# Performance work log

Hardware: AMD Instinct MI355X
Metric: run time of the kernel (lower is better)

The kernel has to match this reference:

```python
import jax, jax.numpy as jnp
import numpy as np

B, LQ, LK, D = 16, 32, 256, 512
H, DK = 8, 64
LN_EPS = 1e-5


def _layernorm(x, g, b):
    m = jnp.mean(x, axis=-1, keepdims=True)
    var = jnp.mean(jnp.square(x - m), axis=-1, keepdims=True)
    return (x - m) * jax.lax.rsqrt(var + LN_EPS) * g + b


def setup_inputs() -> dict:
    key = jax.random.key(0)
    ks = jax.random.split(key, 10)
    s = 0.02
    return {
        "q": jax.random.normal(ks[0], (B, LQ, D), jnp.float32),
        "k": jax.random.normal(ks[1], (B, LK, D), jnp.float32),
        "v": jax.random.normal(ks[2], (B, LK, D), jnp.float32),
        "Wq": jax.random.normal(ks[3], (D, D), jnp.float32) * s,
        "Wk": jax.random.normal(ks[4], (D, D), jnp.float32) * s,
        "Wv": jax.random.normal(ks[5], (D, D), jnp.float32) * s,
        "Wfc": jax.random.normal(ks[6], (D, D), jnp.float32) * s,
        "Wg": jax.random.normal(ks[7], (2 * D, D), jnp.float32) * s,
        "bg": jnp.zeros((2 * D,), jnp.float32),
        "Wvp": jax.random.normal(ks[8], (D, D), jnp.float32) * s,
        "bvp": jnp.zeros((D,), jnp.float32),
        "ln1_g": jnp.ones((D,), jnp.float32),
        "ln1_b": jnp.zeros((D,), jnp.float32),
        "ln2_g": jnp.ones((D,), jnp.float32),
        "ln2_b": jnp.zeros((D,), jnp.float32),
    }


def reference(q, k, v, Wq, Wk, Wv, Wfc, Wg, bg, Wvp, bvp, ln1_g, ln1_b, ln2_g, ln2_b):
    # FiLM parameters from queries: [B, LQ, 2D] -> tanh gammas/betas [B, LQ, D]
    film = q @ Wg.T + bg
    gammas, betas = jnp.split(film, 2, axis=-1)
    gammas = jnp.tanh(gammas)
    betas = jnp.tanh(betas)
    # Visual conditioning base: LN(vis_proj(k)) -> [B, LK, D]
    cond_base = _layernorm(k @ Wvp.T + bvp, ln1_g, ln1_b)
    # Per-query modulated keys: broadcast instead of repeat -> [B, LQ, LK, D]
    cond = gammas[:, :, None, :] * cond_base[:, None, :, :] + betas[:, :, None, :]
    cond_k = k[:, None, :, :] + _layernorm(cond, ln2_g, ln2_b)
    # Projections (torch Linear: y = x @ W^T), no qkv bias
    qh = (q @ Wq.T).reshape(B, LQ, H, DK)                 # [B, LQ, H, DK]
    kh = (cond_k @ Wk.T).reshape(B, LQ, LK, H, DK)        # [B, LQ, LK, H, DK]
    vh = (cond_k @ Wv.T).reshape(B, LQ, LK, H, DK)
    # Per-query attention over LK (note: forward arg `v` is unused, as in original)
    scale = DK ** (-0.5)
    logits = jnp.einsum("blhd,blkhd->bhlk", qh, kh) * scale
    weights = jax.nn.softmax(logits, axis=-1)
    # attn_drop/proj_drop are identity in eval mode
    attn = jnp.einsum("bhlk,blkhd->blhd", weights, vh).reshape(B, LQ, H * DK)
    return attn @ Wfc.T
```

## Files before the change

### kernel.cpp

```cpp
#include <hip/hip_runtime.h>
#include <math.h>

namespace {
constexpr float LN_EPS = 1e-5f;

typedef unsigned short u16;
typedef __attribute__((ext_vector_type(8))) short bh8;
typedef __attribute__((ext_vector_type(4))) float fv4;

__device__ __forceinline__ float4 ld4(const float* p) { return *reinterpret_cast<const float4*>(p); }

__device__ __forceinline__ float b2f(u16 x) {
  union { float f; unsigned u; } c; c.u = ((unsigned)x) << 16; return c.f;
}
__device__ __forceinline__ u16 f2b(float f) {
  union { float f; unsigned u; } c; c.f = f;
  unsigned u = c.u;
  u += 0x7FFFu + ((u >> 16) & 1u);
  return (u16)(u >> 16);
}
__device__ __forceinline__ unsigned pk2(float a, float b) {
  return (unsigned)f2b(a) | ((unsigned)f2b(b) << 16);
}
__device__ __forceinline__ uint4 pack8(const float* v) {
  uint4 r; r.x = pk2(v[0], v[1]); r.y = pk2(v[2], v[3]); r.z = pk2(v[4], v[5]); r.w = pk2(v[6], v[7]);
  return r;
}

__device__ __forceinline__ bh8 lds_rd(const u16* S, int row, int c8) {
  return *(const bh8*)&S[row * 64 + ((c8 ^ (row & 7)) << 3)];
}

struct FA {
  const float *q, *k, *Wq, *Wk, *Wv, *Wfc, *Wg, *bg, *Wvp, *bvp;
  const float *ln1g, *ln1b, *ln2g, *ln2b;
  float* out;
  u16 *WkT_bf, *Wv_bf, *Wfc_bf, *k_bf, *kT_bf, *qh_bf;
  float *gam, *bet, *condpre;
  u16 *cb_bf, *cbT_bf, *u_bf, *w1_bf;
  float *c2, *c3, *c4;
  u16* A96_bf;
  float *sum_be, *sum_be2, *P;
  u16* s_bf;
  u16 *cbsq_bf, *w_bf, *W1_bf;
  float *S1, *S2;
  u16* attn_bf;
  float *K1, *K2;
};

struct GA {
  const u16* A; const u16* B; const u16* Balt;
  long lda, ldb, sAz, sBz;
  float* Cf; u16* Cb; u16* Cb2;
  long ldc, sCz;
  int M, K, epi;
  const float* e0; const float* e1;
};

__device__ __forceinline__ void gemm_core(const GA& a, u16* As, u16* Bs,
                                          int bx, int by, int bz, int t) {
  const int z = bz;
  const int bm0 = bx * 64, bn0 = by * 64;
  const int lane = t & 63, w = t >> 6;
  const int wm = (w >> 1) * 32, wn = (w & 1) * 32;
  const u16* Ab = a.A + (long)z * a.sAz;
  const u16* Bbase = (a.Balt != nullptr && bm0 >= 64) ? a.Balt : a.B;
  const u16* Bb = Bbase + (long)z * a.sBz;

  const int sr = t >> 3, sc8 = t & 7, sc = sc8 * 8;
  int ar0 = bm0 + sr;      if (ar0 > a.M - 1) ar0 = a.M - 1;
  int ar1 = bm0 + sr + 32; if (ar1 > a.M - 1) ar1 = a.M - 1;
  const u16* ap0 = Ab + (long)ar0 * a.lda + sc;
  const u16* ap1 = Ab + (long)ar1 * a.lda + sc;
  const u16* bp0 = Bb + (long)(bn0 + sr) * a.ldb + sc;
  const u16* bp1 = Bb + (long)(bn0 + sr + 32) * a.ldb + sc;
  const int iA0 = sr * 64 + ((sc8 ^ (sr & 7)) << 3);
  const int iA1 = iA0 + 32 * 64;

  fv4 zero = {0.f, 0.f, 0.f, 0.f};
  fv4 acc00 = zero, acc01 = zero, acc10 = zero, acc11 = zero;
  const int r0 = lane & 15, kq8 = lane >> 4;
  const int nk = a.K >> 6;

  uint4 av0 = *(const uint4*)ap0, av1 = *(const uint4*)ap1;
  uint4 bv0 = *(const uint4*)bp0, bv1 = *(const uint4*)bp1;
  for (int kt = 0; kt < nk; ++kt) {
    __syncthreads();
    *(uint4*)&As[iA0] = av0; *(uint4*)&As[iA1] = av1;
    *(uint4*)&Bs[iA0] = bv0; *(uint4*)&Bs[iA1] = bv1;
    __syncthreads();
    if (kt + 1 < nk) {
      ap0 += 64; ap1 += 64; bp0 += 64; bp1 += 64;
      av0 = *(const uint4*)ap0; av1 = *(const uint4*)ap1;
      bv0 = *(const uint4*)bp0; bv1 = *(const uint4*)bp1;
    }
#pragma unroll
    for (int kc = 0; kc < 2; ++kc) {
      const int c8 = kq8 + 4 * kc;
      bh8 aa0 = lds_rd(As, wm + r0, c8);
      bh8 aa1 = lds_rd(As, wm + 16 + r0, c8);
      bh8 bb0 = lds_rd(Bs, wn + r0, c8);
      bh8 bb1 = lds_rd(Bs, wn + 16 + r0, c8);
      acc00 = __builtin_amdgcn_mfma_f32_16x16x32_bf16(aa0, bb0, acc00, 0, 0, 0);
      acc01 = __builtin_amdgcn_mfma_f32_16x16x32_bf16(aa0, bb1, acc01, 0, 0, 0);
      acc10 = __builtin_amdgcn_mfma_f32_16x16x32_bf16(aa1, bb0, acc10, 0, 0, 0);
      acc11 = __builtin_amdgcn_mfma_f32_16x16x32_bf16(aa1, bb1, acc11, 0, 0, 0);
    }
  }

  fv4 accs[2][2] = {{acc00, acc01}, {acc10, acc11}};
#pragma unroll
  for (int rb = 0; rb < 2; ++rb) {
#pragma unroll
    for (int cbl = 0; cbl < 2; ++cbl) {
#pragma unroll
      for (int j = 0; j < 4; ++j) {
        const int r = bm0 + wm + rb * 16 + (lane >> 4) * 4 + j;
        const int c = bn0 + wn + cbl * 16 + (lane & 15);
        if (r >= a.M) continue;
        const float v = accs[rb][cbl][j];
        if (a.epi == 0) {
          a.Cf[(long)z * a.sCz + (long)r * a.ldc + c] = v;
        } else if (a.epi == 1) {
          a.Cb[(long)z * a.sCz + (long)r * a.ldc + c] = f2b(v);
        } else if (a.epi == 5) {
          a.Cb[((long)r * 8 + z) * a.ldc + c] = f2b(v * 0.125f);
        } else {
          const u16 ub = f2b(v * 0.125f);
          const long orow = (long)r * 8 + z;
          a.Cb[orow * 512 + c] = ub;
          const float uu = b2f(ub);
          const float t1 = a.e1[c] * uu;
          a.Cb2[orow * 512 + c] = f2b(a.e0[(long)r * 512 + c] * t1);
        }
      }
    }
  }
}

struct GAF {
  const float* Af; const float* Bf;
  long lda, ldb;
  float* Cf; u16* Cb; float* Cf2;
  long ldc;
  int M, K, epi;
  const float* e0;
};

__device__ __forceinline__ void gemm_core_f32(const GAF& a, u16* As, u16* Bs,
                                              int bx, int by, int t) {
  const int bm0 = bx * 64, bn0 = by * 64;
  const int lane = t & 63, w = t >> 6;
  const int wm = (w >> 1) * 32, wn = (w & 1) * 32;
  const int sr = t >> 3, sc8 = t & 7, sc = sc8 * 8;
  int ar0 = bm0 + sr;      if (ar0 > a.M - 1) ar0 = a.M - 1;
  int ar1 = bm0 + sr + 32; if (ar1 > a.M - 1) ar1 = a.M - 1;
  const float* ap0 = a.Af + (long)ar0 * a.lda + sc;
  const float* ap1 = a.Af + (long)ar1 * a.lda + sc;
  const float* bp0 = a.Bf + (long)(bn0 + sr) * a.ldb + sc;
  const float* bp1 = a.Bf + (long)(bn0 + sr + 32) * a.ldb + sc;
  const int iA0 = sr * 64 + ((sc8 ^ (sr & 7)) << 3);
  const int iA1 = iA0 + 32 * 64;

  fv4 zero = {0.f, 0.f, 0.f, 0.f};
  fv4 acc00 = zero, acc01 = zero, acc10 = zero, acc11 = zero;
  const int r0 = lane & 15, kq8 = lane >> 4;
  const int nk = a.K >> 6;

  float4 xa0 = ld4(ap0), xa1 = ld4(ap0 + 4), xa2 = ld4(ap1), xa3 = ld4(ap1 + 4);
  float4 xb0 = ld4(bp0), xb1 = ld4(bp0 + 4), xb2 = ld4(bp1), xb3 = ld4(bp1 + 4);
  for (int kt = 0; kt < nk; ++kt) {
    __syncthreads();
    {
      const float v0[8] = {xa0.x, xa0.y, xa0.z, xa0.w, xa1.x, xa1.y, xa1.z, xa1.w};
      const float v1[8] = {xa2.x, xa2.y, xa2.z, xa2.w, xa3.x, xa3.y, xa3.z, xa3.w};
      const float v2[8] = {xb0.x, xb0.y, xb0.z, xb0.w, xb1.x, xb1.y, xb1.z, xb1.w};
      const float v3[8] = {xb2.x, xb2.y, xb2.z, xb2.w, xb3.x, xb3.y, xb3.z, xb3.w};
      *(uint4*)&As[iA0] = pack8(v0);
      *(uint4*)&As[iA1] = pack8(v1);
      *(uint4*)&Bs[iA0] = pack8(v2);
      *(uint4*)&Bs[iA1] = pack8(v3);
    }
    __syncthreads();
    if (kt + 1 < nk) {
      ap0 += 64; ap1 += 64; bp0 += 64; bp1 += 64;
      xa0 = ld4(ap0); xa1 = ld4(ap0 + 4); xa2 = ld4(ap1); xa3 = ld4(ap1 + 4);
      xb0 = ld4(bp0); xb1 = ld4(bp0 + 4); xb2 = ld4(bp1); xb3 = ld4(bp1 + 4);
    }
#pragma unroll
    for (int kc = 0; kc < 2; ++kc) {
      const int c8 = kq8 + 4 * kc;
      bh8 aa0 = lds_rd(As, wm + r0, c8);
      bh8 aa1 = lds_rd(As, wm + 16 + r0, c8);
      bh8 bb0 = lds_rd(Bs, wn + r0, c8);
      bh8 bb1 = lds_rd(Bs, wn + 16 + r0, c8);
      acc00 = __builtin_amdgcn_mfma_f32_16x16x32_bf16(aa0, bb0, acc00, 0, 0, 0);
      acc01 = __builtin_amdgcn_mfma_f32_16x16x32_bf16(aa0, bb1, acc01, 0, 0, 0);
      acc10 = __builtin_amdgcn_mfma_f32_16x16x32_bf16(aa1, bb0, acc10, 0, 0, 0);
      acc11 = __builtin_amdgcn_mfma_f32_16x16x32_bf16(aa1, bb1, acc11, 0, 0, 0);
    }
  }

  fv4 accs[2][2] = {{acc00, acc01}, {acc10, acc11}};
#pragma unroll
  for (int rb = 0; rb < 2; ++rb) {
#pragma unroll
    for (int cbl = 0; cbl < 2; ++cbl) {
#pragma unroll
      for (int j = 0; j < 4; ++j) {
        const int r = bm0 + wm + rb * 16 + (lane >> 4) * 4 + j;
        const int c = bn0 + wn + cbl * 16 + (lane & 15);
        if (r >= a.M) continue;
        const float v = accs[rb][cbl][j];
        if (a.epi == 1) {
          a.Cb[(long)r * a.ldc + c] = f2b(v);
        } else if (a.epi == 2) {
          const float x = tanhf(v + a.e0[c]);
          if (c < 512) a.Cf[(long)r * 512 + c] = x;
          else         a.Cf2[(long)r * 512 + (c - 512)] = x;
        } else {
          a.Cf[(long)r * a.ldc + c] = v + a.e0[c];
        }
      }
    }
  }
}

struct GA2 {
  const u16* A1; const u16* A2; const u16* B1; const u16* B2;
  long lda, ldb, sAz, sBz;
  float* Cf; float* Cf2; u16* Cb;
  long ldc, sCz;
  int M, K;
  const float* e1; const float* e2; const float* e3;
  const float* e4; const float* e5; const float* e6;
};

__device__ __forceinline__ void gemm2_core(const GA2& a, u16* As1, u16* As2,
                                           u16* Bs1, u16* Bs2,
                                           int bx, int by, int bz, int t, int EPI) {
  const int z = bz;
  const int bm0 = bx * 64, bn0 = by * 64;
  const int lane = t & 63, w = t >> 6;
  const int wm = (w >> 1) * 32, wn = (w & 1) * 32;
  const u16* A1b = a.A1 + (long)z * a.sAz;
  const u16* A2b = a.A2 + (long)z * a.sAz;
  const u16* B1b = a.B1 + (long)z * a.sBz;
  const u16* B2b = a.B2 + (long)z * a.sBz;

  const int sr = t >> 3, sc8 = t & 7, sc = sc8 * 8;
  const long aoff0 = (long)(bm0 + sr) * a.lda + sc;
  const long aoff1 = (long)(bm0 + sr + 32) * a.lda + sc;
  const long boff0 = (long)(bn0 + sr) * a.ldb + sc;
  const long boff1 = (long)(bn0 + sr + 32) * a.ldb + sc;
  const u16 *a1p0 = A1b + aoff0, *a1p1 = A1b + aoff1;
  const u16 *a2p0 = A2b + aoff0, *a2p1 = A2b + aoff1;
  const u16 *b1p0 = B1b + boff0, *b1p1 = B1b + boff1;
  const u16 *b2p0 = B2b + boff0, *b2p1 = B2b + boff1;
  const int iA0 = sr * 64 + ((sc8 ^ (sr & 7)) << 3);
  const int iA1 = iA0 + 32 * 64;

  fv4 zero = {0.f, 0.f, 0.f, 0.f};
  fv4 p00 = zero, p01 = zero, p10 = zero, p11 = zero;
  fv4 q00 = zero, q01 = zero, q10 = zero, q11 = zero;
  const int r0 = lane & 15, kq8 = lane >> 4;
  const int nk = a.K >> 6;

  uint4 a1v0 = *(const uint4*)a1p0, a1v1 = *(const uint4*)a1p1;
  uint4 a2v0 = *(const uint4*)a2p0, a2v1 = *(const uint4*)a2p1;
  uint4 b1v0 = *(const uint4*)b1p0, b1v1 = *(const uint4*)b1p1;
  uint4 b2v0 = *(const uint4*)b2p0, b2v1 = *(const uint4*)b2p1;
  for (int kt = 0; kt < nk; ++kt) {
    __syncthreads();
    *(uint4*)&As1[iA0] = a1v0; *(uint4*)&As1[iA1] = a1v1;
    *(uint4*)&As2[iA0] = a2v0; *(uint4*)&As2[iA1] = a2v1;
    *(uint4*)&Bs1[iA0] = b1v0; *(uint4*)&Bs1[iA1] = b1v1;
    *(uint4*)&Bs2[iA0] = b2v0; *(uint4*)&Bs2[iA1] = b2v1;
    __syncthreads();
    if (kt + 1 < nk) {
      a1p0 += 64; a1p1 += 64; a2p0 += 64; a2p1 += 64;
      b1p0 += 64; b1p1 += 64; b2p0 += 64; b2p1 += 64;
      a1v0 = *(const uint4*)a1p0; a1v1 = *(const uint4*)a1p1;
      a2v0 = *(const uint4*)a2p0; a2v1 = *(const uint4*)a2p1;
      b1v0 = *(const uint4*)b1p0; b1v1 = *(const uint4*)b1p1;
      b2v0 = *(const uint4*)b2p0; b2v1 = *(const uint4*)b2p1;
    }
#pragma unroll
    for (int kc = 0; kc < 2; ++kc) {
      const int c8 = kq8 + 4 * kc;
      bh8 x0 = lds_rd(As1, wm + r0, c8);
      bh8 x1 = lds_rd(As1, wm + 16 + r0, c8);
      bh8 y0 = lds_rd(Bs1, wn + r0, c8);
      bh8 y1 = lds_rd(Bs1, wn + 16 + r0, c8);
      p00 = __builtin_amdgcn_mfma_f32_16x16x32_bf16(x0, y0, p00, 0, 0, 0);
      p01 = __builtin_amdgcn_mfma_f32_16x16x32_bf16(x0, y1, p01, 0, 0, 0);
      p10 = __builtin_amdgcn_mfma_f32_16x16x32_bf16(x1, y0, p10, 0, 0, 0);
      p11 = __builtin_amdgcn_mfma_f32_16x16x32_bf16(x1, y1, p11, 0, 0, 0);
      bh8 u0 = lds_rd(As2, wm + r0, c8);
      bh8 u1 = lds_rd(As2, wm + 16 + r0, c8);
      bh8 v0 = lds_rd(Bs2, wn + r0, c8);
      bh8 v1 = lds_rd(Bs2, wn + 16 + r0, c8);
      q00 = __builtin_amdgcn_mfma_f32_16x16x32_bf16(u0, v0, q00, 0, 0, 0);
      q01 = __builtin_amdgcn_mfma_f32_16x16x32_bf16(u0, v1, q01, 0, 0, 0);
      q10 = __builtin_amdgcn_mfma_f32_16x16x32_bf16(u1, v0, q10, 0, 0, 0);
      q11 = __builtin_amdgcn_mfma_f32_16x16x32_bf16(u1, v1, q11, 0, 0, 0);
    }
  }

  fv4 pa[2][2] = {{p00, p01}, {p10, p11}};
  fv4 qa[2][2] = {{q00, q01}, {q10, q11}};
#pragma unroll
  for (int rb = 0; rb < 2; ++rb) {
#pragma unroll
    for (int cbl = 0; cbl < 2; ++cbl) {
#pragma unroll
      for (int j = 0; j < 4; ++j) {
        const int r = bm0 + wm + rb * 16 + (lane >> 4) * 4 + j;
        const int c = bn0 + wn + cbl * 16 + (lane & 15);
        if (r >= a.M) continue;
        const float v1 = pa[rb][cbl][j];
        const float v2 = qa[rb][cbl][j];
        if (EPI == 2) {
          const long idx = (long)z * a.sCz + (long)r * a.ldc + c;
          a.Cf[idx] = v1;
          a.Cf2[idx] = v2;
        } else {
          const int lh = z * 256 + r;
          const int bl = z * 32 + (r >> 3);
          const float G2d = a.e1[c], B2d = a.e2[c];
          const float gv = a.e3[(long)bl * 512 + c];
          const float bev = a.e4[(long)bl * 512 + c];
          const float sv = v1 + B2d + G2d * (gv * v2 + bev * a.e5[lh] - a.e6[lh]);
          a.Cb[(long)z * a.sCz + (long)r * a.ldc + c] = f2b(sv);
        }
      }
    }
  }
}

__device__ __forceinline__ void tpf32_unit(const float* src, long lds, u16* dst, long ldd,
                                           int tr, int tc, int t, float T[64][65]) {
  const int c = t & 63, rg = t >> 6;
#pragma unroll 4
  for (int i = 0; i < 16; ++i) {
    const int r = rg + 4 * i;
    T[r][c] = src[(long)(tr * 64 + r) * lds + tc * 64 + c];
  }
  __syncthreads();
#pragma unroll 4
  for (int i = 0; i < 16; ++i) {
    const int r = rg + 4 * i;
    dst[(long)(tc * 64 + r) * ldd + tr * 64 + c] = f2b(T[c][r]);
  }
}

__device__ __forceinline__ void tpb16_unit(const u16* src, u16* dst, int b, int w32,
                                           int t, float T[64][65]) {
  const int tr = w32 >> 3, tc = w32 & 7;
  const u16* s = src + (long)b * 131072;
  u16* d = dst + (long)b * 131072;
  const int c = t & 63, rg = t >> 6;
#pragma unroll 4
  for (int i = 0; i < 16; ++i) {
    const int r = rg + 4 * i;
    T[r][c] = b2f(s[(long)(tr * 64 + r) * 512 + tc * 64 + c]);
  }
  __syncthreads();
#pragma unroll 4
  for (int i = 0; i < 16; ++i) {
    const int r = rg + 4 * i;
    d[(long)(tc * 64 + r) * 256 + tr * 64 + c] = f2b(T[c][r]);
  }
}

__device__ __forceinline__ void cvt_unit(const float* s, u16* d, long blk, int t) {
  const long idx = blk * 2048 + t * 8;
  const float4 x0 = ld4(s + idx), x1 = ld4(s + idx + 4);
  const float v[8] = {x0.x, x0.y, x0.z, x0.w, x1.x, x1.y, x1.z, x1.w};
  *(uint4*)(d + idx) = pack8(v);
}

__device__ __forceinline__ void ln_unit(const FA& f, int u, int t) {
  const int lane = t & 63, e = lane * 8;
  const int row = u * 4 + (t >> 6);
  const float* p = f.condpre + (long)row * 512 + e;
  const float4 x0 = ld4(p), x1 = ld4(p + 4);
  float v[8] = {x0.x, x0.y, x0.z, x0.w, x1.x, x1.y, x1.z, x1.w};
  float s = 0.f, sq = 0.f;
#pragma unroll
  for (int i = 0; i < 8; ++i) { s += v[i]; sq += v[i] * v[i]; }
#pragma unroll
  for (int m = 1; m < 64; m <<= 1) { s += __shfl_xor(s, m); sq += __shfl_xor(sq, m); }
  const float mu = s * (1.f / 512.f);
  const float iv = rsqrtf(sq * (1.f / 512.f) - mu * mu + LN_EPS);
  const float4 g0 = ld4(f.ln1g + e), g1 = ld4(f.ln1g + e + 4);
  const float4 b0 = ld4(f.ln1b + e), b1 = ld4(f.ln1b + e + 4);
  const float gg[8] = {g0.x, g0.y, g0.z, g0.w, g1.x, g1.y, g1.z, g1.w};
  const float bb[8] = {b0.x, b0.y, b0.z, b0.w, b1.x, b1.y, b1.z, b1.w};
  float o[8], osq[8];
#pragma unroll
  for (int i = 0; i < 8; ++i) {
    o[i] = (v[i] - mu) * iv * gg[i] + bb[i];
    osq[i] = o[i] * o[i];
  }
  *(uint4*)(f.cb_bf + (long)row * 512 + e) = pack8(o);
  *(uint4*)(f.cbsq_bf + (long)row * 512 + e) = pack8(osq);
}

__device__ __forceinline__ void a96_unit(const FA& f, int u, int t) {
  const int lane = t & 63, e = lane * 8;
  const int bl = u * 4 + (t >> 6);
  const int b = bl >> 5, l = bl & 31;
  const float4 ga0 = ld4(f.gam + (long)bl * 512 + e), ga1 = ld4(f.gam + (long)bl * 512 + e + 4);
  const float4 be0 = ld4(f.bet + (long)bl * 512 + e), be1 = ld4(f.bet + (long)bl * 512 + e + 4);
  const float gv[8] = {ga0.x, ga0.y, ga0.z, ga0.w, ga1.x, ga1.y, ga1.z, ga1.w};
  const float bv[8] = {be0.x, be0.y, be0.z, be0.w, be1.x, be1.y, be1.z, be1.w};
  float gg[8], gb[8]; float s1 = 0.f, s2 = 0.f;
#pragma unroll
  for (int i = 0; i < 8; ++i) {
    gg[i] = gv[i] * gv[i]; gb[i] = gv[i] * bv[i];
    s1 += bv[i]; s2 += bv[i] * bv[i];
  }
  const long basei = ((long)b * 96 + l) * 512 + e;
  *(uint4*)(f.A96_bf + basei) = pack8(gv);
  *(uint4*)(f.A96_bf + basei + 32 * 512) = pack8(gb);
  *(uint4*)(f.A96_bf + basei + 64 * 512) = pack8(gg);
#pragma unroll
  for (int m = 1; m < 64; m <<= 1) { s1 += __shfl_xor(s1, m); s2 += __shfl_xor(s2, m); }
  if (lane == 0) { f.sum_be[bl] = s1; f.sum_be2[bl] = s2; }
}

__device__ __forceinline__ void csum_unit(const FA& f, int u, int t) {
  const int lane = t & 63, e = lane * 8;
  const int lh = u * 4 + (t >> 6);
  const int bl = lh >> 3;
  const uint4 up = *(const uint4*)(f.u_bf + (long)lh * 512 + e);
  const u16* us = (const u16*)&up;
  const float4 be0 = ld4(f.bet + (long)bl * 512 + e), be1 = ld4(f.bet + (long)bl * 512 + e + 4);
  const float4 G0 = ld4(f.ln2g + e), G1 = ld4(f.ln2g + e + 4);
  const float4 B0 = ld4(f.ln2b + e), B1 = ld4(f.ln2b + e + 4);
  const float bv[8] = {be0.x, be0.y, be0.z, be0.w, be1.x, be1.y, be1.z, be1.w};
  const float Gv[8] = {G0.x, G0.y, G0.z, G0.w, G1.x, G1.y, G1.z, G1.w};
  const float Bv[8] = {B0.x, B0.y, B0.z, B0.w, B1.x, B1.y, B1.z, B1.w};
  float a2 = 0.f, a3 = 0.f, a4 = 0.f;
#pragma unroll
  for (int i = 0; i < 8; ++i) {
    const float uu = b2f(us[i]);
    const float t1 = Gv[i] * uu;
    a2 += bv[i] * t1; a3 += t1; a4 += Bv[i] * uu;
  }
#pragma unroll
  for (int m = 1; m < 64; m <<= 1) {
    a2 += __shfl_xor(a2, m); a3 += __shfl_xor(a3, m); a4 += __shfl_xor(a4, m);
  }
  if (lane == 0) { f.c2[lh] = a2; f.c3[lh] = a3; f.c4[lh] = a4; }
}

__device__ __forceinline__ void softmax2_unit(const FA& f, int u, int t) {
  const int lane = t & 63, e = lane * 4;
  const int lh = u * 4 + (t >> 6);
  const int b = lh >> 8, l = (lh >> 3) & 31, bl = lh >> 3;
  const float4 k1 = ld4(f.K1 + (long)lh * 256 + e);
  const float4 k2 = ld4(f.K2 + (long)lh * 256 + e);
  const float* Pb = f.P + ((long)b * 96 + l) * 256 + e;
  const float4 p0 = ld4(Pb), pgb = ld4(Pb + 32 * 256), pg2 = ld4(Pb + 64 * 256);
  const float sbe = f.sum_be[bl], sbe2 = f.sum_be2[bl];
  const float C2 = f.c2[lh], C3 = f.c3[lh], C4 = f.c4[lh];
  const float k1s[4] = {k1.x, k1.y, k1.z, k1.w};
  const float k2s[4] = {k2.x, k2.y, k2.z, k2.w};
  const float p0s[4] = {p0.x, p0.y, p0.z, p0.w};
  const float pgbs[4] = {pgb.x, pgb.y, pgb.z, pgb.w};
  const float pg2s[4] = {pg2.x, pg2.y, pg2.z, pg2.w};
  float mu[4], iv[4], lgs[4];
#pragma unroll
  for (int i = 0; i < 4; ++i) {
    mu[i] = (p0s[i] + sbe) * (1.f / 512.f);
    const float msq = (pg2s[i] + 2.f * pgbs[i] + sbe2) * (1.f / 512.f);
    iv[i] = rsqrtf(msq - mu[i] * mu[i] + LN_EPS);
    lgs[i] = k1s[i] + C4 + iv[i] * (k2s[i] + C2 - mu[i] * C3);
  }
  float mx = fmaxf(fmaxf(lgs[0], lgs[1]), fmaxf(lgs[2], lgs[3]));
#pragma unroll
  for (int m = 1; m < 64; m <<= 1) mx = fmaxf(mx, __shfl_xor(mx, m));
  float ex[4]; float z = 0.f;
#pragma unroll
  for (int i = 0; i < 4; ++i) { ex[i] = expf(lgs[i] - mx); z += ex[i]; }
#pragma unroll
  for (int m = 1; m < 64; m <<= 1) z += __shfl_xor(z, m);
  const float rz = 1.f / z;
  float wv[4], w1v[4]; float s1 = 0.f, s2 = 0.f;
#pragma unroll
  for (int i = 0; i < 4; ++i) {
    wv[i] = ex[i] * rz;
    w1v[i] = wv[i] * iv[i];
    s1 += w1v[i]; s2 += w1v[i] * mu[i];
  }
  uint2 wp, w1p;
  wp.x = pk2(wv[0], wv[1]); wp.y = pk2(wv[2], wv[3]);
  w1p.x = pk2(w1v[0], w1v[1]); w1p.y = pk2(w1v[2], w1v[3]);
  *(uint2*)(f.w_bf + (long)lh * 256 + e) = wp;
  *(uint2*)(f.W1_bf + (long)lh * 256 + e) = w1p;
#pragma unroll
  for (int m = 1; m < 64; m <<= 1) { s1 += __shfl_xor(s1, m); s2 += __shfl_xor(s2, m); }
  if (lane == 0) { f.S1[lh] = s1; f.S2[lh] = s2; }
}

__global__ __launch_bounds__(256) void pA_k(FA f) {
  __shared__ __align__(16) char smem[16704];
  u16* As = (u16*)smem;
  u16* Bs = (u16*)(smem + 8192);
  float (*T)[65] = (float(*)[65])smem;
  const int u = blockIdx.x, t = threadIdx.x;
  if (u < 512) {
    GAF a = {}; a.Af = f.k; a.Bf = f.Wvp; a.lda = 512; a.ldb = 512;
    a.Cf = f.condpre; a.ldc = 512; a.M = 4096; a.K = 512; a.epi = 4; a.e0 = f.bvp;
    gemm_core_f32(a, As, Bs, u % 64, u / 64, t);
  } else if (u < 640) {
    const int r = u - 512;
    GAF a = {}; a.Af = f.q; a.Bf = f.Wg; a.lda = 512; a.ldb = 512;
    a.Cf = f.gam; a.Cf2 = f.bet; a.ldc = 512; a.M = 512; a.K = 512; a.epi = 2; a.e0 = f.bg;
    gemm_core_f32(a, As, Bs, r % 8, r / 8, t);
  } else if (u < 704) {
    const int r = u - 640;
    GAF a = {}; a.Af = f.q; a.Bf = f.Wq; a.lda = 512; a.ldb = 512;
    a.Cb = f.qh_bf; a.ldc = 512; a.M = 512; a.K = 512; a.epi = 1;
    gemm_core_f32(a, As, Bs, r % 8, r / 8, t);
  } else if (u < 1728) {
    cvt_unit(f.k, f.k_bf, u - 704, t);
  } else if (u < 1856) {
    cvt_unit(f.Wv, f.Wv_bf, u - 1728, t);
  } else if (u < 1984) {
    cvt_unit(f.Wfc, f.Wfc_bf, u - 1856, t);
  } else if (u < 2048) {
    const int tt = u - 1984;
    tpf32_unit(f.Wk, 512, f.WkT_bf, 512, tt >> 3, tt & 7, t, T);
  } else {
    const int tt = u - 2048;
    const int b = tt >> 5, w32 = tt & 31;
    tpf32_unit(f.k + (long)b * 131072, 512, f.kT_bf + (long)b * 131072, 256,
               w32 >> 3, w32 & 7, t, T);
  }
}

__global__ __launch_bounds__(256) void pB_k(FA f) {
  __shared__ __align__(16) char smem[16384];
  u16* As = (u16*)smem;
  u16* Bs = (u16*)(smem + 8192);
  const int u = blockIdx.x, t = threadIdx.x;
  if (u < 1024) {
    ln_unit(f, u, t);
  } else if (u < 1152) {
    a96_unit(f, u - 1024, t);
  } else {
    const int r = u - 1152;
    GA a = {}; a.A = f.qh_bf; a.lda = 512; a.sAz = 64;
    a.B = f.WkT_bf; a.ldb = 512; a.sBz = 64;
    a.Cb = f.u_bf; a.Cb2 = f.w1_bf; a.ldc = 512; a.M = 512; a.K = 64; a.epi = 6;
    a.e0 = f.gam; a.e1 = f.ln2g;
    gemm_core(a, As, Bs, r % 8, (r / 8) % 8, r / 64, t);
  }
}

__global__ __launch_bounds__(256) void pC_k(FA f) {
  __shared__ __align__(16) char smem[32768];
  const int u = blockIdx.x, t = threadIdx.x;
  if (u < 128) {
    u16* As = (u16*)smem; u16* Bs = (u16*)(smem + 8192);
    GA a = {}; a.A = f.A96_bf; a.lda = 512; a.sAz = 96 * 512;
    a.B = f.cb_bf; a.Balt = f.cbsq_bf; a.ldb = 512; a.sBz = 256 * 512;
    a.Cf = f.P; a.ldc = 256; a.sCz = 96 * 256; a.M = 96; a.K = 512; a.epi = 0;
    gemm_core(a, As, Bs, u % 2, (u / 2) % 4, u / 8, t);
  } else if (u < 640) {
    float (*T)[65] = (float(*)[65])smem;
    const int tt = u - 128;
    tpb16_unit(f.cb_bf, f.cbT_bf, tt >> 5, tt & 31, t, T);
  } else if (u < 1664) {
    csum_unit(f, u - 640, t);
  } else {
    const int r = u - 1664;
    u16* As1 = (u16*)smem; u16* As2 = (u16*)(smem + 8192);
    u16* Bs1 = (u16*)(smem + 16384); u16* Bs2 = (u16*)(smem + 24576);
    GA2 d = {};
    d.A1 = f.u_bf; d.A2 = f.w1_bf; d.B1 = f.k_bf; d.B2 = f.cb_bf;
    d.lda = 512; d.ldb = 512; d.sAz = 256 * 512; d.sBz = 256 * 512;
    d.Cf = f.K1; d.Cf2 = f.K2; d.ldc = 256; d.sCz = 256 * 256; d.M = 256; d.K = 512;
    gemm2_core(d, As1, As2, Bs1, Bs2, r % 4, (r / 4) % 4, r / 16, t, 2);
  }
}

__global__ __launch_bounds__(256) void pD_k(FA f) {
  softmax2_unit(f, blockIdx.x, threadIdx.x);
}

__global__ __launch_bounds__(256) void pE_k(FA f) {
  __shared__ __align__(16) char smem[32768];
  u16* As1 = (u16*)smem; u16* As2 = (u16*)(smem + 8192);
  u16* Bs1 = (u16*)(smem + 16384); u16* Bs2 = (u16*)(smem + 24576);
  const int u = blockIdx.x, t = threadIdx.x;
  GA2 d = {};
  d.A1 = f.w_bf; d.A2 = f.W1_bf; d.B1 = f.kT_bf; d.B2 = f.cbT_bf;
  d.lda = 256; d.ldb = 256; d.sAz = 256 * 256; d.sBz = 512 * 256;
  d.Cb = f.s_bf; d.ldc = 512; d.sCz = 256 * 512; d.M = 256; d.K = 256;
  d.e1 = f.ln2g; d.e2 = f.ln2b; d.e3 = f.gam; d.e4 = f.bet; d.e5 = f.S1; d.e6 = f.S2;
  gemm2_core(d, As1, As2, Bs1, Bs2, u % 4, (u / 4) % 8, u / 32, t, 1);
}

__global__ __launch_bounds__(256) void pF_k(FA f) {
  __shared__ __align__(16) char smem[16384];
  u16* As = (u16*)smem; u16* Bs = (u16*)(smem + 8192);
  const int u = blockIdx.x, t = threadIdx.x;
  GA a = {}; a.A = f.s_bf; a.lda = 4096; a.sAz = 512;
  a.B = f.Wv_bf; a.ldb = 512; a.sBz = 64 * 512;
  a.Cb = f.attn_bf; a.ldc = 512; a.sCz = 64; a.M = 512; a.K = 512; a.epi = 1;
  gemm_core(a, As, Bs, u % 8, 0, u / 8, t);
}

__global__ __launch_bounds__(256) void pG_k(FA f) {
  __shared__ __align__(16) char smem[16384];
  u16* As = (u16*)smem; u16* Bs = (u16*)(smem + 8192);
  const int u = blockIdx.x, t = threadIdx.x;
  GA a = {}; a.A = f.attn_bf; a.lda = 512;
  a.B = f.Wfc_bf; a.ldb = 512;
  a.Cf = f.out; a.ldc = 512; a.M = 512; a.K = 512; a.epi = 0;
  gemm_core(a, As, Bs, u % 8, u / 8, 0, t);
}

}

extern "C" void kernel_launch(void* const* d_in, const int* in_sizes, int n_in,
                              void* d_out, int out_size, void* d_ws, size_t ws_size,
                              hipStream_t stream) {
  (void)in_sizes; (void)n_in; (void)out_size;
  FA fa;
  fa.q    = (const float*)d_in[0];
  fa.k    = (const float*)d_in[1];
  fa.Wq   = (const float*)d_in[3];
  fa.Wk   = (const float*)d_in[4];
  fa.Wv   = (const float*)d_in[5];
  fa.Wfc  = (const float*)d_in[6];
  fa.Wg   = (const float*)d_in[7];
  fa.bg   = (const float*)d_in[8];
  fa.Wvp  = (const float*)d_in[9];
  fa.bvp  = (const float*)d_in[10];
  fa.ln1g = (const float*)d_in[11];
  fa.ln1b = (const float*)d_in[12];
  fa.ln2g = (const float*)d_in[13];
  fa.ln2b = (const float*)d_in[14];
  fa.out  = (float*)d_out;

  char* base = (char*)d_ws;
  size_t off = 0;
  auto au16 = [&](size_t n) -> u16* {
    u16* p = (u16*)(base + off); off = (off + n * 2 + 255) & ~(size_t)255; return p;
  };
  auto af32 = [&](size_t n) -> float* {
    float* p = (float*)(base + off); off = (off + n * 4 + 255) & ~(size_t)255; return p;
  };
  (void)au16(262144);
  (void)au16(524288);
  (void)au16(262144);
  (void)au16(262144);
  fa.WkT_bf  = au16(262144);
  fa.Wv_bf   = au16(262144);
  fa.Wfc_bf  = au16(262144);
  fa.k_bf    = au16(2097152);
  fa.kT_bf   = au16(2097152);
  fa.qh_bf   = au16(262144);
  fa.gam     = af32(262144);
  fa.bet     = af32(262144);
  fa.condpre = af32(2097152);
  fa.cb_bf   = au16(2097152);
  fa.cbT_bf  = au16(2097152);
  fa.u_bf    = au16(2097152);
  fa.w1_bf   = au16(2097152);
  fa.c2      = af32(4096);
  fa.c3      = af32(4096);
  fa.c4      = af32(4096);
  fa.A96_bf  = au16(16 * 96 * 512);
  fa.sum_be  = af32(512);
  fa.sum_be2 = af32(512);
  fa.P       = af32(16 * 96 * 256);
  float* sbuf   = af32(1048576);
  float* logits = af32(1048576);
  fa.w_bf    = au16(1048576);
  fa.W1_bf   = au16(1048576);
  fa.S1      = af32(4096);
  fa.S2      = af32(4096);
  fa.attn_bf = au16(262144);
  const size_t need = off;
  fa.s_bf    = (u16*)sbuf;
  fa.cbsq_bf = (u16*)logits;
  fa.K1      = fa.condpre;
  fa.K2      = fa.condpre + 1048576;

  if (ws_size < need) return;

  const dim3 blk(256);
  pA_k<<<dim3(2560), blk, 0, stream>>>(fa);
  pB_k<<<dim3(1664), blk, 0, stream>>>(fa);
  pC_k<<<dim3(1920), blk, 0, stream>>>(fa);
  pD_k<<<dim3(1024), blk, 0, stream>>>(fa);
  pE_k<<<dim3(512),  blk, 0, stream>>>(fa);
  pF_k<<<dim3(64),   blk, 0, stream>>>(fa);
  pG_k<<<dim3(64),   blk, 0, stream>>>(fa);
}
```

Baseline: 82.29 us.

## Use larger GEMM tiles for vis_proj and dual-GEMM stages

Replaces the 64x64 fp32-input GEMM for the k@Wvp projection with a new 128x128 tile kernel, where each wave computes a 64x64 sub-tile with 16 MFMA accumulators. The dual-GEMM core is widened from 64x64 to 64x128 output tiles. Grid sizes and shared-memory allocations are adjusted to match. Larger tiles raise operand reuse and cut redundant global loads, at the cost of fewer blocks, more registers and more LDS per block, which lowers occupancy. The new fp32 kernel also drops the software prefetch of the next k-tile.

```diff
diff --git a/kernel.cpp b/kernel.cpp
--- a/kernel.cpp
+++ b/kernel.cpp
@@ -226,6 +226,74 @@
   }
 }
 
+struct G128 {
+  const float* Af; const float* Bf;
+  long lda, ldb;
+  float* Cf;
+  long ldc;
+  int K;
+  const float* bias;
+};
+
+__device__ __forceinline__ void gemm128_f32(const G128& a, u16* As, u16* Bs,
+                                            int bx, int by, int t) {
+  const int bm0 = bx * 128, bn0 = by * 128;
+  const int lane = t & 63, w = t >> 6;
+  const int qm = (w >> 1) * 64, qn = (w & 1) * 64;
+  const int srb = t >> 3, sc8 = t & 7;
+  const int r0 = lane & 15, kq8 = lane >> 4;
+  const int nk = a.K >> 6;
+  const int slot = (sc8 ^ (srb & 7)) << 3;
+
+  fv4 acc[4][4];
+#pragma unroll
+  for (int mi = 0; mi < 4; ++mi)
+#pragma unroll
+    for (int ni = 0; ni < 4; ++ni) acc[mi][ni] = {0.f, 0.f, 0.f, 0.f};
+
+  for (int kt = 0; kt < nk; ++kt) {
+    __syncthreads();
+    const long kof = (long)kt * 64 + sc8 * 8;
+#pragma unroll
+    for (int i = 0; i < 4; ++i) {
+      const int r = i * 32 + srb;
+      const float* pa = a.Af + (long)(bm0 + r) * a.lda + kof;
+      const float4 x0 = ld4(pa), x1 = ld4(pa + 4);
+      const float va[8] = {x0.x, x0.y, x0.z, x0.w, x1.x, x1.y, x1.z, x1.w};
+      *(uint4*)&As[r * 64 + slot] = pack8(va);
+      const float* pb = a.Bf + (long)(bn0 + r) * a.ldb + kof;
+      const float4 y0 = ld4(pb), y1 = ld4(pb + 4);
+      const float vb[8] = {y0.x, y0.y, y0.z, y0.w, y1.x, y1.y, y1.z, y1.w};
+      *(uint4*)&Bs[r * 64 + slot] = pack8(vb);
+    }
+    __syncthreads();
+#pragma unroll
+    for (int kc = 0; kc < 2; ++kc) {
+      const int c8 = kq8 + 4 * kc;
+      bh8 af[4], bf[4];
+#pragma unroll
+      for (int mi = 0; mi < 4; ++mi) af[mi] = lds_rd(As, qm + mi * 16 + r0, c8);
+#pragma unroll
+      for (int ni = 0; ni < 4; ++ni) bf[ni] = lds_rd(Bs, qn + ni * 16 + r0, c8);
+#pragma unroll
+      for (int mi = 0; mi < 4; ++mi)
+#pragma unroll
+        for (int ni = 0; ni < 4; ++ni)
+          acc[mi][ni] = __builtin_amdgcn_mfma_f32_16x16x32_bf16(af[mi], bf[ni], acc[mi][ni], 0, 0, 0);
+    }
+  }
+#pragma unroll
+  for (int mi = 0; mi < 4; ++mi)
+#pragma unroll
+    for (int ni = 0; ni < 4; ++ni)
+#pragma unroll
+      for (int j = 0; j < 4; ++j) {
+        const int r = bm0 + qm + mi * 16 + (lane >> 4) * 4 + j;
+        const int c = bn0 + qn + ni * 16 + (lane & 15);
+        a.Cf[(long)r * a.ldc + c] = acc[mi][ni][j] + a.bias[c];
+      }
+}
+
 struct GA2 {
   const u16* A1; const u16* A2; const u16* B1; const u16* B2;
   long lda, ldb, sAz, sBz;
@@ -236,90 +304,103 @@
   const float* e4; const float* e5; const float* e6;
 };
 
-__device__ __forceinline__ void gemm2_core(const GA2& a, u16* As1, u16* As2,
-                                           u16* Bs1, u16* Bs2,
-                                           int bx, int by, int bz, int t, int EPI) {
+__device__ __forceinline__ void gemm2w_core(const GA2& a, u16* As1, u16* As2,
+                                            u16* Bs1, u16* Bs2,
+                                            int bx, int by, int bz, int t, int EPI) {
   const int z = bz;
-  const int bm0 = bx * 64, bn0 = by * 64;
+  const int bm0 = bx * 64, bn0 = by * 128;
   const int lane = t & 63, w = t >> 6;
-  const int wm = (w >> 1) * 32, wn = (w & 1) * 32;
+  const int wm = (w >> 1) * 32, wn = (w & 1) * 64;
   const u16* A1b = a.A1 + (long)z * a.sAz;
   const u16* A2b = a.A2 + (long)z * a.sAz;
   const u16* B1b = a.B1 + (long)z * a.sBz;
   const u16* B2b = a.B2 + (long)z * a.sBz;
 
-  const int sr = t >> 3, sc8 = t & 7, sc = sc8 * 8;
-  const long aoff0 = (long)(bm0 + sr) * a.lda + sc;
-  const long aoff1 = (long)(bm0 + sr + 32) * a.lda + sc;
-  const long boff0 = (long)(bn0 + sr) * a.ldb + sc;
-  const long boff1 = (long)(bn0 + sr + 32) * a.ldb + sc;
-  const u16 *a1p0 = A1b + aoff0, *a1p1 = A1b + aoff1;
-  const u16 *a2p0 = A2b + aoff0, *a2p1 = A2b + aoff1;
-  const u16 *b1p0 = B1b + boff0, *b1p1 = B1b + boff1;
-  const u16 *b2p0 = B2b + boff0, *b2p1 = B2b + boff1;
-  const int iA0 = sr * 64 + ((sc8 ^ (sr & 7)) << 3);
-  const int iA1 = iA0 + 32 * 64;
-
-  fv4 zero = {0.f, 0.f, 0.f, 0.f};
-  fv4 p00 = zero, p01 = zero, p10 = zero, p11 = zero;
-  fv4 q00 = zero, q01 = zero, q10 = zero, q11 = zero;
+  const int srb = t >> 3, sc8 = t & 7, sc = sc8 * 8;
+  const int slot = (sc8 ^ (srb & 7)) << 3;
+  const int iA0 = srb * 64 + slot, iA1 = iA0 + 32 * 64;
+  const u16* a1p0 = A1b + (long)(bm0 + srb) * a.lda + sc;
+  const u16* a1p1 = A1b + (long)(bm0 + srb + 32) * a.lda + sc;
+  const u16* a2p0 = A2b + (long)(bm0 + srb) * a.lda + sc;
+  const u16* a2p1 = A2b + (long)(bm0 + srb + 32) * a.lda + sc;
+  const u16* b1p[4]; const u16* b2p[4];
+#pragma unroll
+  for (int i = 0; i < 4; ++i) {
+    b1p[i] = B1b + (long)(bn0 + i * 32 + srb) * a.ldb + sc;
+    b2p[i] = B2b + (long)(bn0 + i * 32 + srb) * a.ldb + sc;
+  }
+
+  fv4 p[2][4], q[2][4];
+#pragma unroll
+  for (int mi = 0; mi < 2; ++mi)
+#pragma unroll
+    for (int ni = 0; ni < 4; ++ni) { p[mi][ni] = {0.f,0.f,0.f,0.f}; q[mi][ni] = {0.f,0.f,0.f,0.f}; }
+
   const int r0 = lane & 15, kq8 = lane >> 4;
   const int nk = a.K >> 6;
 
   uint4 a1v0 = *(const uint4*)a1p0, a1v1 = *(const uint4*)a1p1;
   uint4 a2v0 = *(const uint4*)a2p0, a2v1 = *(const uint4*)a2p1;
-  uint4 b1v0 = *(const uint4*)b1p0, b1v1 = *(const uint4*)b1p1;
-  uint4 b2v0 = *(const uint4*)b2p0, b2v1 = *(const uint4*)b2p1;
+  uint4 b1v[4], b2v[4];
+#pragma unroll
+  for (int i = 0; i < 4; ++i) { b1v[i] = *(const uint4*)b1p[i]; b2v[i] = *(const uint4*)b2p[i]; }
+
   for (int kt = 0; kt < nk; ++kt) {
     __syncthreads();
     *(uint4*)&As1[iA0] = a1v0; *(uint4*)&As1[iA1] = a1v1;
     *(uint4*)&As2[iA0] = a2v0; *(uint4*)&As2[iA1] = a2v1;
-    *(uint4*)&Bs1[iA0] = b1v0; *(uint4*)&Bs1[iA1] = b1v1;
-    *(uint4*)&Bs2[iA0] = b2v0; *(uint4*)&Bs2[iA1] = b2v1;
+#pragma unroll
+    for (int i = 0; i < 4; ++i) {
+      *(uint4*)&Bs1[iA0 + i * 2048] = b1v[i];
+      *(uint4*)&Bs2[iA0 + i * 2048] = b2v[i];
+    }
     __syncthreads();
     if (kt + 1 < nk) {
       a1p0 += 64; a1p1 += 64; a2p0 += 64; a2p1 += 64;
-      b1p0 += 64; b1p1 += 64; b2p0 += 64; b2p1 += 64;
       a1v0 = *(const uint4*)a1p0; a1v1 = *(const uint4*)a1p1;
       a2v0 = *(const uint4*)a2p0; a2v1 = *(const uint4*)a2p1;
-      b1v0 = *(const uint4*)b1p0; b1v1 = *(const uint4*)b1p1;
-      b2v0 = *(const uint4*)b2p0; b2v1 = *(const uint4*)b2p1;
+#pragma unroll
+      for (int i = 0; i < 4; ++i) {
+        b1p[i] += 64; b2p[i] += 64;
+        b1v[i] = *(const uint4*)b1p[i]; b2v[i] = *(const uint4*)b2p[i];
+      }
     }
 #pragma unroll
     for (int kc = 0; kc < 2; ++kc) {
       const int c8 = kq8 + 4 * kc;
       bh8 x0 = lds_rd(As1, wm + r0, c8);
       bh8 x1 = lds_rd(As1, wm + 16 + r0, c8);
-      bh8 y0 = lds_rd(Bs1, wn + r0, c8);
-      bh8 y1 = lds_rd(Bs1, wn + 16 + r0, c8);
-      p00 = __builtin_amdgcn_mfma_f32_16x16x32_bf16(x0, y0, p00, 0, 0, 0);
-      p01 = __builtin_amdgcn_mfma_f32_16x16x32_bf16(x0, y1, p01, 0, 0, 0);
-      p10 = __builtin_amdgcn_mfma_f32_16x16x32_bf16(x1, y0, p10, 0, 0, 0);
-      p11 = __builtin_amdgcn_mfma_f32_16x16x32_bf16(x1, y1, p11, 0, 0, 0);
+      bh8 y[4];
+#pragma unroll
+      for (int ni = 0; ni < 4; ++ni) y[ni] = lds_rd(Bs1, wn + ni * 16 + r0, c8);
+#pragma unroll
+      for (int ni = 0; ni < 4; ++ni) {
+        p[0][ni] = __builtin_amdgcn_mfma_f32_16x16x32_bf16(x0, y[ni], p[0][ni], 0, 0, 0);
+        p[1][ni] = __builtin_amdgcn_mfma_f32_16x16x32_bf16(x1, y[ni], p[1][ni], 0, 0, 0);
+      }
       bh8 u0 = lds_rd(As2, wm + r0, c8);
       bh8 u1 = lds_rd(As2, wm + 16 + r0, c8);
-      bh8 v0 = lds_rd(Bs2, wn + r0, c8);
-      bh8 v1 = lds_rd(Bs2, wn + 16 + r0, c8);
-      q00 = __builtin_amdgcn_mfma_f32_16x16x32_bf16(u0, v0, q00, 0, 0, 0);
-      q01 = __builtin_amdgcn_mfma_f32_16x16x32_bf16(u0, v1, q01, 0, 0, 0);
-      q10 = __builtin_amdgcn_mfma_f32_16x16x32_bf16(u1, v0, q10, 0, 0, 0);
-      q11 = __builtin_amdgcn_mfma_f32_16x16x32_bf16(u1, v1, q11, 0, 0, 0);
-    }
-  }
-
-  fv4 pa[2][2] = {{p00, p01}, {p10, p11}};
-  fv4 qa[2][2] = {{q00, q01}, {q10, q11}};
-#pragma unroll
-  for (int rb = 0; rb < 2; ++rb) {
-#pragma unroll
-    for (int cbl = 0; cbl < 2; ++cbl) {
+      bh8 v[4];
+#pragma unroll
+      for (int ni = 0; ni < 4; ++ni) v[ni] = lds_rd(Bs2, wn + ni * 16 + r0, c8);
+#pragma unroll
+      for (int ni = 0; ni < 4; ++ni) {
+        q[0][ni] = __builtin_amdgcn_mfma_f32_16x16x32_bf16(u0, v[ni], q[0][ni], 0, 0, 0);
+        q[1][ni] = __builtin_amdgcn_mfma_f32_16x16x32_bf16(u1, v[ni], q[1][ni], 0, 0, 0);
+      }
+    }
+  }
+
+#pragma unroll
+  for (int mi = 0; mi < 2; ++mi)
+#pragma unroll
+    for (int ni = 0; ni < 4; ++ni)
 #pragma unroll
       for (int j = 0; j < 4; ++j) {
-        const int r = bm0 + wm + rb * 16 + (lane >> 4) * 4 + j;
-        const int c = bn0 + wn + cbl * 16 + (lane & 15);
-        if (r >= a.M) continue;
-        const float v1 = pa[rb][cbl][j];
-        const float v2 = qa[rb][cbl][j];
+        const int r = bm0 + wm + mi * 16 + (lane >> 4) * 4 + j;
+        const int c = bn0 + wn + ni * 16 + (lane & 15);
+        const float v1 = p[mi][ni][j];
+        const float v2 = q[mi][ni][j];
         if (EPI == 2) {
           const long idx = (long)z * a.sCz + (long)r * a.ldc + c;
           a.Cf[idx] = v1;
@@ -334,8 +415,6 @@
           a.Cb[(long)z * a.sCz + (long)r * a.ldc + c] = f2b(sv);
         }
       }
-    }
-  }
 }
 
 __device__ __forceinline__ void tpf32_unit(const float* src, long lds, u16* dst, long ldd,
@@ -506,36 +585,37 @@
 }
 
 __global__ __launch_bounds__(256) void pA_k(FA f) {
-  __shared__ __align__(16) char smem[16704];
-  u16* As = (u16*)smem;
-  u16* Bs = (u16*)(smem + 8192);
+  __shared__ __align__(16) char smem[32768];
   float (*T)[65] = (float(*)[65])smem;
   const int u = blockIdx.x, t = threadIdx.x;
-  if (u < 512) {
-    GAF a = {}; a.Af = f.k; a.Bf = f.Wvp; a.lda = 512; a.ldb = 512;
-    a.Cf = f.condpre; a.ldc = 512; a.M = 4096; a.K = 512; a.epi = 4; a.e0 = f.bvp;
-    gemm_core_f32(a, As, Bs, u % 64, u / 64, t);
-  } else if (u < 640) {
-    const int r = u - 512;
+  if (u < 128) {
+    u16* As = (u16*)smem; u16* Bs = (u16*)(smem + 16384);
+    G128 a = {}; a.Af = f.k; a.Bf = f.Wvp; a.lda = 512; a.ldb = 512;
+    a.Cf = f.condpre; a.ldc = 512; a.K = 512; a.bias = f.bvp;
+    gemm128_f32(a, As, Bs, u % 32, u / 32, t);
+  } else if (u < 256) {
+    u16* As = (u16*)smem; u16* Bs = (u16*)(smem + 8192);
+    const int r = u - 128;
     GAF a = {}; a.Af = f.q; a.Bf = f.Wg; a.lda = 512; a.ldb = 512;
     a.Cf = f.gam; a.Cf2 = f.bet; a.ldc = 512; a.M = 512; a.K = 512; a.epi = 2; a.e0 = f.bg;
     gemm_core_f32(a, As, Bs, r % 8, r / 8, t);
-  } else if (u < 704) {
-    const int r = u - 640;
+  } else if (u < 320) {
+    u16* As = (u16*)smem; u16* Bs = (u16*)(smem + 8192);
+    const int r = u - 256;
     GAF a = {}; a.Af = f.q; a.Bf = f.Wq; a.lda = 512; a.ldb = 512;
     a.Cb = f.qh_bf; a.ldc = 512; a.M = 512; a.K = 512; a.epi = 1;
     gemm_core_f32(a, As, Bs, r % 8, r / 8, t);
-  } else if (u < 1728) {
-    cvt_unit(f.k, f.k_bf, u - 704, t);
-  } else if (u < 1856) {
-    cvt_unit(f.Wv, f.Wv_bf, u - 1728, t);
-  } else if (u < 1984) {
-    cvt_unit(f.Wfc, f.Wfc_bf, u - 1856, t);
-  } else if (u < 2048) {
-    const int tt = u - 1984;
+  } else if (u < 1344) {
+    cvt_unit(f.k, f.k_bf, u - 320, t);
+  } else if (u < 1472) {
+    cvt_unit(f.Wv, f.Wv_bf, u - 1344, t);
+  } else if (u < 1600) {
+    cvt_unit(f.Wfc, f.Wfc_bf, u - 1472, t);
+  } else if (u < 1664) {
+    const int tt = u - 1600;
     tpf32_unit(f.Wk, 512, f.WkT_bf, 512, tt >> 3, tt & 7, t, T);
   } else {
-    const int tt = u - 2048;
+    const int tt = u - 1664;
     const int b = tt >> 5, w32 = tt & 31;
     tpf32_unit(f.k + (long)b * 131072, 512, f.kT_bf + (long)b * 131072, 256,
                w32 >> 3, w32 & 7, t, T);
@@ -562,7 +642,7 @@
 }
 
 __global__ __launch_bounds__(256) void pC_k(FA f) {
-  __shared__ __align__(16) char smem[32768];
+  __shared__ __align__(16) char smem[49152];
   const int u = blockIdx.x, t = threadIdx.x;
   if (u < 128) {
     u16* As = (u16*)smem; u16* Bs = (u16*)(smem + 8192);
@@ -579,12 +659,12 @@
   } else {
     const int r = u - 1664;
     u16* As1 = (u16*)smem; u16* As2 = (u16*)(smem + 8192);
-    u16* Bs1 = (u16*)(smem + 16384); u16* Bs2 = (u16*)(smem + 24576);
+    u16* Bs1 = (u16*)(smem + 16384); u16* Bs2 = (u16*)(smem + 32768);
     GA2 d = {};
     d.A1 = f.u_bf; d.A2 = f.w1_bf; d.B1 = f.k_bf; d.B2 = f.cb_bf;
     d.lda = 512; d.ldb = 512; d.sAz = 256 * 512; d.sBz = 256 * 512;
     d.Cf = f.K1; d.Cf2 = f.K2; d.ldc = 256; d.sCz = 256 * 256; d.M = 256; d.K = 512;
-    gemm2_core(d, As1, As2, Bs1, Bs2, r % 4, (r / 4) % 4, r / 16, t, 2);
+    gemm2w_core(d, As1, As2, Bs1, Bs2, r % 4, (r / 4) % 2, r / 8, t, 2);
   }
 }
 
@@ -593,16 +673,16 @@
 }
 
 __global__ __launch_bounds__(256) void pE_k(FA f) {
-  __shared__ __align__(16) char smem[32768];
+  __shared__ __align__(16) char smem[49152];
   u16* As1 = (u16*)smem; u16* As2 = (u16*)(smem + 8192);
-  u16* Bs1 = (u16*)(smem + 16384); u16* Bs2 = (u16*)(smem + 24576);
+  u16* Bs1 = (u16*)(smem + 16384); u16* Bs2 = (u16*)(smem + 32768);
   const int u = blockIdx.x, t = threadIdx.x;
   GA2 d = {};
   d.A1 = f.w_bf; d.A2 = f.W1_bf; d.B1 = f.kT_bf; d.B2 = f.cbT_bf;
   d.lda = 256; d.ldb = 256; d.sAz = 256 * 256; d.sBz = 512 * 256;
   d.Cb = f.s_bf; d.ldc = 512; d.sCz = 256 * 512; d.M = 256; d.K = 256;
   d.e1 = f.ln2g; d.e2 = f.ln2b; d.e3 = f.gam; d.e4 = f.bet; d.e5 = f.S1; d.e6 = f.S2;
-  gemm2_core(d, As1, As2, Bs1, Bs2, u % 4, (u / 4) % 8, u / 32, t, 1);
+  gemm2w_core(d, As1, As2, Bs1, Bs2, u % 4, (u / 4) % 4, u / 16, t, 1);
 }
 
 __global__ __launch_bounds__(256) void pF_k(FA f) {
@@ -696,11 +776,11 @@
   if (ws_size < need) return;
 
   const dim3 blk(256);
-  pA_k<<<dim3(2560), blk, 0, stream>>>(fa);
+  pA_k<<<dim3(2176), blk, 0, stream>>>(fa);
   pB_k<<<dim3(1664), blk, 0, stream>>>(fa);
-  pC_k<<<dim3(1920), blk, 0, stream>>>(fa);
+  pC_k<<<dim3(1792), blk, 0, stream>>>(fa);
   pD_k<<<dim3(1024), blk, 0, stream>>>(fa);
-  pE_k<<<dim3(512),  blk, 0, stream>>>(fa);
+  pE_k<<<dim3(256),  blk, 0, stream>>>(fa);
   pF_k<<<dim3(64),   blk, 0, stream>>>(fa);
   pG_k<<<dim3(64),   blk, 0, stream>>>(fa);
 }
```

After: 121.5 us. +47.6%, slower.
